# Optimization experiments

Hardware: AMD Instinct MI355X
Metric: run time of the kernel (lower is better)

## Reference

```python
import jax, jax.numpy as jnp
import numpy as np

D_MODEL = 128
D_STATE = 64
D_CONV = 4
EXPAND = 2
HEADDIM = 64
NUM_LAYERS = 2
N_DIR = 6
D_INNER = EXPAND * D_MODEL                    # 256
NHEADS = D_INNER // HEADDIM                   # 4
CONV_DIM = D_INNER + 2 * D_STATE              # 384
D_PROJ = 2 * D_INNER + 2 * D_STATE + NHEADS   # 644
ORDERS = [(0, 1, 2), (0, 2, 1), (1, 0, 2), (1, 2, 0), (2, 0, 1), (2, 1, 0)]


def setup_inputs() -> dict:
    key = jax.random.key(0)
    ks = jax.random.split(key, 10)
    B, L = 1, 16384
    sh = (N_DIR, NUM_LAYERS)
    return {
        'vectors': jax.random.normal(ks[0], (B, L, D_MODEL), jnp.float32),
        'event_coords': jax.random.randint(ks[1], (L, 4), 0, 1024, jnp.int32),
        'ln_w': jnp.ones(sh + (D_MODEL,), jnp.float32),
        'ln_b': jnp.zeros(sh + (D_MODEL,), jnp.float32),
        'in_w': 0.05 * jax.random.normal(ks[2], sh + (D_PROJ, D_MODEL), jnp.float32),
        'conv_w': 0.1 * jax.random.normal(ks[3], sh + (CONV_DIM, D_CONV), jnp.float32),
        'conv_b': jnp.zeros(sh + (CONV_DIM,), jnp.float32),
        'dt_bias': 0.1 * jax.random.normal(ks[4], sh + (NHEADS,), jnp.float32),
        'A_log': jnp.log(jax.random.uniform(ks[5], sh + (NHEADS,), jnp.float32, 1.0, 16.0)),
        'D_skip': jnp.ones(sh + (NHEADS,), jnp.float32),
        'norm_w': jnp.ones(sh + (D_INNER,), jnp.float32),
        'out_w': 0.05 * jax.random.normal(ks[6], sh + (D_MODEL, D_INNER), jnp.float32),
        'fuse_ln_w': jnp.ones((N_DIR * D_MODEL,), jnp.float32),
        'fuse_ln_b': jnp.zeros((N_DIR * D_MODEL,), jnp.float32),
        'fuse_w': 0.05 * jax.random.normal(ks[7], (D_MODEL, N_DIR * D_MODEL), jnp.float32),
        'fuse_b': jnp.zeros((D_MODEL,), jnp.float32),
    }


def _layernorm(x, w, b, eps=1e-5):
    mu = jnp.mean(x, -1, keepdims=True)
    var = jnp.mean((x - mu) ** 2, -1, keepdims=True)
    return (x - mu) * jax.lax.rsqrt(var + eps) * w + b


def _mamba2(x, in_w, conv_w, conv_b, dt_bias, A_log, D_skip, norm_w, out_w):
    # x: [b, l, d_model] -> [b, l, d_model]; Mamba2 (ngroups=1, headdim=64)
    b, l, _ = x.shape
    zxbcdt = jnp.einsum('bld,ed->ble', x, in_w)      # [b,l,644]
    z = zxbcdt[..., :D_INNER]                        # gate [b,l,256]
    xBC = zxbcdt[..., D_INNER:D_INNER + CONV_DIM]    # [b,l,384]
    dt = jax.nn.softplus(zxbcdt[..., D_INNER + CONV_DIM:] + dt_bias)  # [b,l,h]
    # causal depthwise conv over time, then SiLU
    xc = jnp.transpose(xBC, (0, 2, 1))               # [b,c,l]
    xc = jax.lax.conv_general_dilated(
        xc, conv_w[:, None, :], (1,), [(D_CONV - 1, 0)],
        feature_group_count=CONV_DIM, dimension_numbers=('NCH', 'OIH', 'NCH'))
    xBC = jax.nn.silu(jnp.transpose(xc, (0, 2, 1)) + conv_b)
    xs = xBC[..., :D_INNER].reshape(b, l, NHEADS, HEADDIM)   # [b,l,h,p]
    Bm = xBC[..., D_INNER:D_INNER + D_STATE]                 # [b,l,n]
    Cm = xBC[..., D_INNER + D_STATE:]                        # [b,l,n]
    A = -jnp.exp(A_log)                                      # [h]
    dA = jnp.exp(dt * A)                                     # [b,l,h]
    dtx = dt[..., None] * xs                                 # [b,l,h,p]

    def step(h, inp):
        dA_t, dtx_t, B_t, C_t = inp
        h = dA_t[:, :, None, None] * h + dtx_t[..., None] * B_t[:, None, None, :]
        y = jnp.einsum('bn,bhpn->bhp', C_t, h)
        return h, y

    h0 = jnp.zeros((b, NHEADS, HEADDIM, D_STATE), x.dtype)
    _, ys = jax.lax.scan(step, h0, (
        jnp.moveaxis(dA, 1, 0), jnp.moveaxis(dtx, 1, 0),
        jnp.moveaxis(Bm, 1, 0), jnp.moveaxis(Cm, 1, 0)))
    y = jnp.moveaxis(ys, 0, 1) + D_skip[None, None, :, None] * xs  # [b,l,h,p]
    y = y.reshape(b, l, D_INNER)
    # gated RMSNorm (norm_before_gate=False): gate first, then RMSNorm
    y = y * jax.nn.silu(z)
    y = y * jax.lax.rsqrt(jnp.mean(y * y, -1, keepdims=True) + 1e-5) * norm_w
    return jnp.einsum('ble,de->bld', y, out_w)


def _forward(vectors, event_coords, ln_w, ln_b, in_w, conv_w, conv_b, dt_bias,
             A_log, D_skip, norm_w, out_w, fuse_ln_w, fuse_ln_b, fuse_w, fuse_b):
    outs = []
    for d, axes in enumerate(ORDERS):
        keys = [event_coords[:, ax] for ax in reversed(axes)]
        idx = jnp.lexsort(keys)            # lexsort: last key is primary
        inv = jnp.argsort(idx)
        x = vectors[:, idx, :]
        for j in range(NUM_LAYERS):
            x = x + _mamba2(_layernorm(x, ln_w[d, j], ln_b[d, j]),
                            in_w[d, j], conv_w[d, j], conv_b[d, j],
                            dt_bias[d, j], A_log[d, j], D_skip[d, j],
                            norm_w[d, j], out_w[d, j])
        outs.append(x[:, inv, :])
    multi = jnp.concatenate(outs, -1)      # [b,l,6*d_model]
    h = _layernorm(multi, fuse_ln_w, fuse_ln_b)
    h = jnp.einsum('ble,de->bld', h, fuse_w) + fuse_b
    return jax.nn.gelu(h, approximate=False)


def reference(vectors, event_coords, ln_w, ln_b, in_w, conv_w, conv_b, dt_bias,
              A_log, D_skip, norm_w, out_w, fuse_ln_w, fuse_ln_b, fuse_w, fuse_b):
    return _forward(vectors, event_coords, ln_w, ln_b, in_w, conv_w, conv_b,
                    dt_bias, A_log, D_skip, norm_w, out_w,
                    fuse_ln_w, fuse_ln_b, fuse_w, fuse_b)
```

## Files before the change

kernel.cpp:

```cpp
#include <hip/hip_runtime.h>
#include <math.h>

#define LSEQ   16384
#define DM     128
#define DI     256
#define DSTATE 64
#define NH     4
#define HD     64
#define CONVD  384
#define DPROJ  644
#define NDIR   6
#define NCHUNK 256

typedef unsigned short u16;
typedef __attribute__((ext_vector_type(8))) __bf16 bf16x8;
typedef __attribute__((ext_vector_type(4))) float f32x4;

union U8 { uint4 v; u16 h[8]; };

__device__ __constant__ int ORD[6][3] = {{0,1,2},{0,2,1},{1,0,2},{1,2,0},{2,0,1},{2,1,0}};

__device__ __forceinline__ float softplus_f(float x){
  float ax = fabsf(x);
  return fmaxf(x, 0.f) + log1pf(__expf(-ax));
}
__device__ __forceinline__ float silu_f(float x){
  return x / (1.f + __expf(-x));
}
__device__ __forceinline__ u16 f2b(float f){
  unsigned u = __float_as_uint(f);
  unsigned r = (u + 0x7fffu + ((u >> 16) & 1u)) >> 16;
  return (u16)r;
}
__device__ __forceinline__ float b2f(u16 h){
  return __uint_as_float(((unsigned)h) << 16);
}
__device__ __forceinline__ int SWZ(int r, int cb){
  return r*128 + (cb ^ ((r & 7) << 4));
}
__device__ __forceinline__ int SWZ2(int r, int cb){
  return r*256 + (cb ^ ((r & 7) << 4));
}
__device__ __forceinline__ int SWZ4(int r, int cb){
  return r*512 + (cb ^ ((r & 7) << 4));
}

#define NW0 (12*768*128)
#define NW1 (12*128*256)
#define NW2 (128*768)
__global__ __launch_bounds__(256) void k_cvt(const float* __restrict__ in_w,
                                             const float* __restrict__ out_w,
                                             const float* __restrict__ fuse_w,
                                             u16* __restrict__ wi, u16* __restrict__ wo,
                                             u16* __restrict__ wf, int* __restrict__ cursor){
  int i = blockIdx.x*256 + threadIdx.x;
  if (i < NDIR*1024) cursor[i] = 0;
  if (i < NW0){
    int dj = i / (768*128), rem = i % (768*128), r = rem >> 7, c = rem & 127;
    float v = (r < DPROJ) ? in_w[((size_t)dj*DPROJ + r)*128 + c] : 0.f;
    wi[i] = f2b(v);
  } else if (i < NW0 + NW1){
    int k = i - NW0;
    wo[k] = f2b(out_w[k]);
  } else if (i < NW0 + NW1 + NW2){
    int k = i - NW0 - NW1;
    wf[k] = f2b(fuse_w[k]);
  }
}

__global__ __launch_bounds__(256) void k_sort1(const int* __restrict__ coords,
                                               unsigned long long* __restrict__ skey,
                                               int* __restrict__ cursor){
  int i = blockIdx.x*256 + threadIdx.x;
  if (i >= NDIR*LSEQ) return;
  int d = i >> 14, t = i & 16383;
  unsigned k = ((unsigned)coords[t*4 + ORD[d][0]] << 20)
             | ((unsigned)coords[t*4 + ORD[d][1]] << 10)
             |  (unsigned)coords[t*4 + ORD[d][2]];
  skey[i] = ((unsigned long long)k << 14) | (unsigned long long)t;
  atomicAdd(&cursor[(d << 10) + (k >> 20)], 1);
}

__global__ void k_sort_scan(int* __restrict__ cursor, int* __restrict__ starts){
  __shared__ int sh[1024];
  int d = blockIdx.x, t = threadIdx.x;
  int v = cursor[d*1024 + t];
  sh[t] = v; __syncthreads();
  for (int off = 1; off < 1024; off <<= 1){
    int a = (t >= off) ? sh[t-off] : 0;
    __syncthreads();
    sh[t] += a;
    __syncthreads();
  }
  int incl = sh[t], excl = incl - v;
  starts[d*1025 + t] = excl;
  cursor[d*1024 + t] = excl;
  if (t == 1023) starts[d*1025 + 1024] = incl;
}

__global__ __launch_bounds__(256) void k_sort_scatter(const unsigned long long* __restrict__ skey,
                                                      unsigned long long* __restrict__ skey2,
                                                      int* __restrict__ cursor){
  int i = blockIdx.x*256 + threadIdx.x;
  if (i >= NDIR*LSEQ) return;
  int d = i >> 14;
  unsigned long long v = skey[i];
  int b = (int)(v >> 34);
  int pos = atomicAdd(&cursor[(d << 10) + b], 1);
  skey2[(size_t)d*LSEQ + pos] = v;
}

__global__ __launch_bounds__(256) void k_sort_rank(const unsigned long long* __restrict__ skey2,
                                                   const int* __restrict__ starts,
                                                   int* __restrict__ idx){
  int i = blockIdx.x*256 + threadIdx.x;
  if (i >= NDIR*LSEQ) return;
  int d = i >> 14;
  unsigned long long v = skey2[i];
  int b = (int)(v >> 34);
  int s = starts[d*1025 + b], e = starts[d*1025 + b + 1];
  int r = s;
  for (int q = s; q < e; ++q) r += (skey2[(size_t)d*LSEQ + q] < v);
  int orig = (int)(v & 16383ULL);
  idx[(size_t)d*LSEQ + r] = orig;
}

__global__ __launch_bounds__(256) void k_gather(const float* __restrict__ vec, const int* __restrict__ idx,
                                                float* __restrict__ x, int d_base, int nd){
  int i = blockIdx.x*256 + threadIdx.x;
  if (i >= nd*LSEQ*32) return;
  int c4 = i & 31, r = (i >> 5) & 16383, dz = i >> 19;
  int src = idx[(size_t)(d_base+dz)*LSEQ + r];
  ((float4*)x)[((size_t)dz*LSEQ + r)*32 + c4] = ((const float4*)vec)[(size_t)src*32 + c4];
}

__global__ __launch_bounds__(256) void k_inproj(const float* __restrict__ xres,
    const float* __restrict__ lnw, const float* __restrict__ lnb,
    const u16* __restrict__ wbf, const float* __restrict__ dt_bias,
    u16* __restrict__ zbuf, u16* __restrict__ xbc, float* __restrict__ dtb,
    int d_base, int j){
  __shared__ __align__(16) u16 As[64*128];
  __shared__ __align__(16) u16 Bs[128*64];
  int bpair = blockIdx.x, mt = blockIdx.y, dz = blockIdx.z, tid = threadIdx.x;
  int dj = (d_base+dz)*2 + j;
  int l = tid & 63, w = tid >> 6, wr = w >> 1, wc = w & 1;
  if (tid < 128){
    int r = tid >> 1, half = tid & 1;
    const float4* xr = (const float4*)(xres + ((size_t)dz*LSEQ + (size_t)mt*64 + r)*DM + half*64);
    float4 v[16];
    #pragma unroll
    for (int q = 0; q < 16; ++q) v[q] = xr[q];
    float s = 0.f, ss2 = 0.f;
    #pragma unroll
    for (int q = 0; q < 16; ++q){
      s   += v[q].x + v[q].y + v[q].z + v[q].w;
      ss2 += v[q].x*v[q].x + v[q].y*v[q].y + v[q].z*v[q].z + v[q].w*v[q].w;
    }
    s += __shfl_xor(s, 1); ss2 += __shfl_xor(ss2, 1);
    float mu = s*(1.f/128.f);
    float var = ss2*(1.f/128.f) - mu*mu;
    float inv = rsqrtf(var + 1e-5f);
    const float4* w4 = (const float4*)(lnw + (size_t)dj*DM) + half*16;
    const float4* b4 = (const float4*)(lnb + (size_t)dj*DM) + half*16;
    #pragma unroll
    for (int g = 0; g < 8; ++g){
      float4 a = v[2*g], b = v[2*g+1];
      float4 wa = w4[2*g], wb = w4[2*g+1];
      float4 ba = b4[2*g], bb = b4[2*g+1];
      U8 pk;
      pk.h[0] = f2b((a.x-mu)*inv*wa.x + ba.x);
      pk.h[1] = f2b((a.y-mu)*inv*wa.y + ba.y);
      pk.h[2] = f2b((a.z-mu)*inv*wa.z + ba.z);
      pk.h[3] = f2b((a.w-mu)*inv*wa.w + ba.w);
      pk.h[4] = f2b((b.x-mu)*inv*wb.x + bb.x);
      pk.h[5] = f2b((b.y-mu)*inv*wb.y + bb.y);
      pk.h[6] = f2b((b.z-mu)*inv*wb.z + bb.z);
      pk.h[7] = f2b((b.w-mu)*inv*wb.w + bb.w);
      int c0 = half*64 + g*8;
      *(uint4*)((char*)As + SWZ2(r, c0*2)) = pk.v;
    }
  }
  __syncthreads();
  for (int ib = 0; ib < 2; ++ib){
    int bn = bpair*2 + ib;
    const u16* Wd = wbf + (size_t)dj*768*DM + (size_t)bn*128*DM;
    f32x4 acc[2][4] = {};
    for (int kt = 0; kt < 2; ++kt){
      #pragma unroll
      for (int it = 0; it < 4; ++it){
        int idx = it*256 + tid, r = idx >> 3, slot = idx & 7;
        uint4 vb = *(const uint4*)(Wd + (size_t)r*DM + kt*64 + slot*8);
        *(uint4*)((char*)Bs + SWZ(r, slot*16)) = vb;
      }
      __syncthreads();
      #pragma unroll
      for (int ks = 0; ks < 64; ks += 32){
        bf16x8 a[2], b[4];
        int cbb = (ks + (l >> 4)*8)*2;
        int kea = kt*64 + ks + (l >> 4)*8;
        #pragma unroll
        for (int i = 0; i < 2; ++i){
          int ra = wr*32 + i*16 + (l & 15);
          a[i] = *(bf16x8*)((char*)As + SWZ2(ra, kea*2));
        }
        #pragma unroll
        for (int i = 0; i < 4; ++i)
          b[i] = *(bf16x8*)((char*)Bs + SWZ(wc*64 + i*16 + (l & 15), cbb));
        #pragma unroll
        for (int i = 0; i < 2; ++i)
          #pragma unroll
          for (int jn = 0; jn < 4; ++jn)
            acc[i][jn] = __builtin_amdgcn_mfma_f32_16x16x32_bf16(a[i], b[jn], acc[i][jn], 0, 0, 0);
      }
      __syncthreads();
    }
    if (bn < 5){
      #pragma unroll
      for (int i = 0; i < 2; ++i)
        #pragma unroll
        for (int jn = 0; jn < 4; ++jn)
          #pragma unroll
          for (int r = 0; r < 4; ++r){
            int m = wr*32 + i*16 + (l >> 4)*4 + r, n = wc*64 + jn*16 + (l & 15);
            Bs[m*128 + n] = f2b(acc[i][jn][r]);
          }
      __syncthreads();
      int co0 = bn*128;
      u16* dst; int ld;
      if (co0 < 256){ dst = zbuf + ((size_t)dz*LSEQ + (size_t)mt*64)*DI + co0; ld = DI; }
      else         { dst = xbc  + ((size_t)dz*LSEQ + (size_t)mt*64)*CONVD + (co0 - 256); ld = CONVD; }
      #pragma unroll
      for (int it = 0; it < 4; ++it){
        int idx = it*256 + tid, r = idx >> 4, slot = idx & 15;
        uint4 v = *(uint4*)(Bs + r*128 + slot*8);
        *(uint4*)(dst + (size_t)r*ld + slot*8) = v;
      }
      __syncthreads();
    } else {
      #pragma unroll
      for (int i = 0; i < 2; ++i)
        #pragma unroll
        for (int jn = 0; jn < 4; ++jn)
          #pragma unroll
          for (int r = 0; r < 4; ++r){
            int m = wr*32 + i*16 + (l >> 4)*4 + r, n = wc*64 + jn*16 + (l & 15);
            if (n < 4){
              float v = acc[i][jn][r] + dt_bias[dj*4 + n];
              dtb[((size_t)dz*LSEQ + (size_t)mt*64 + m)*4 + n] = softplus_f(v);
            }
          }
    }
  }
}

__global__ __launch_bounds__(256) void k_conv(const u16* __restrict__ xbc, const float* __restrict__ conv_w,
                                              const float* __restrict__ conv_b, u16* __restrict__ xact,
                                              int d_base, int j){
  __shared__ float tile[67][130];
  __shared__ float wsh[128][4];
  __shared__ float bsh[128];
  int dz = blockIdx.x, lb = blockIdx.y*64, cb = blockIdx.z*128;
  int dj = (d_base+dz)*2 + j;
  const u16* src = xbc + (size_t)dz*LSEQ*CONVD + cb;
  for (int e = threadIdx.x; e < 67*16; e += 256){
    int r = e >> 4, cg = e & 15;
    int lrow = lb - 3 + r;
    U8 v;
    if (lrow >= 0) v.v = *(const uint4*)(src + (size_t)lrow*CONVD + cg*8);
    else v.v = make_uint4(0,0,0,0);
    #pragma unroll
    for (int k = 0; k < 8; ++k) tile[r][cg*8 + k] = b2f(v.h[k]);
  }
  if (threadIdx.x < 128){
    int c = threadIdx.x;
    const float* wp = conv_w + ((size_t)dj*CONVD + cb + c)*4;
    wsh[c][0]=wp[0]; wsh[c][1]=wp[1]; wsh[c][2]=wp[2]; wsh[c][3]=wp[3];
    bsh[c] = conv_b[(size_t)dj*CONVD + cb + c];
  }
  __syncthreads();
  for (int e = threadIdx.x; e < 64*16; e += 256){
    int r = e >> 4, cg = e & 15;
    U8 o;
    #pragma unroll
    for (int k = 0; k < 8; ++k){
      int c = cg*8 + k;
      float v = tile[r][c]*wsh[c][0] + tile[r+1][c]*wsh[c][1]
              + tile[r+2][c]*wsh[c][2] + tile[r+3][c]*wsh[c][3] + bsh[c];
      o.h[k] = f2b(silu_f(v));
    }
    *(uint4*)(xact + ((size_t)dz*LSEQ + lb + r)*CONVD + cb + cg*8) = o.v;
  }
}

__global__ __launch_bounds__(256) void k_chunk1(const u16* __restrict__ xact, const float* __restrict__ dtb,
    const float* __restrict__ A_log, const float* __restrict__ Dskip,
    u16* __restrict__ E, u16* __restrict__ y1, float* __restrict__ ltot, int d_base, int j){
  __shared__ __align__(16) u16 sB[4096], sC[4096], sM[4096], sXt[4096], sBw[4096];
  __shared__ float sLl[4][64], sdt[4][64];
  __shared__ float wexp[64];
  int c = blockIdx.x, dz = blockIdx.y, tid = threadIdx.x;
  int dj = (d_base+dz)*2 + j;
  int l = tid & 63, w = tid >> 6, wr = w >> 1, wc = w & 1;
  int mb = wr*32, nb = wc*32;
  int row0 = c*64;
  const u16* xa = xact + ((size_t)dz*LSEQ + row0)*CONVD;
  {
    float4 d4 = *(const float4*)(dtb + ((size_t)dz*LSEQ + row0 + l)*4);
    float dt = (w==0)?d4.x:((w==1)?d4.y:((w==2)?d4.z:d4.w));
    float A = -__expf(A_log[dj*4 + w]);
    float v = dt * A;
    #pragma unroll
    for (int o = 1; o < 64; o <<= 1){ float pv = __shfl_up(v, o); if (l >= o) v += pv; }
    sdt[w][l] = dt; sLl[w][l] = v;
    if (l == 63) ltot[((size_t)(dz*NCHUNK + c))*NH + w] = v;
  }
  #pragma unroll
  for (int it = 0; it < 2; ++it){
    int idx = it*256 + tid, t = idx >> 3, slot = idx & 7;
    uint4 vB = *(const uint4*)(xa + (size_t)t*CONVD + 256 + slot*8);
    uint4 vC = *(const uint4*)(xa + (size_t)t*CONVD + 320 + slot*8);
    *(uint4*)((char*)sB + SWZ(t, slot*16)) = vB;
    *(uint4*)((char*)sC + SWZ(t, slot*16)) = vC;
  }
  __syncthreads();
  f32x4 g[2][2] = {};
  #pragma unroll
  for (int ks = 0; ks < 64; ks += 32){
    bf16x8 a[2], b[2];
    int cb = (ks + (l >> 4)*8)*2;
    #pragma unroll
    for (int i = 0; i < 2; ++i){
      a[i] = *(bf16x8*)((char*)sC + SWZ(mb + i*16 + (l & 15), cb));
      b[i] = *(bf16x8*)((char*)sB + SWZ(nb + i*16 + (l & 15), cb));
    }
    #pragma unroll
    for (int i = 0; i < 2; ++i)
      #pragma unroll
      for (int jn = 0; jn < 2; ++jn)
        g[i][jn] = __builtin_amdgcn_mfma_f32_16x16x32_bf16(a[i], b[jn], g[i][jn], 0, 0, 0);
  }
  for (int h = 0; h < NH; ++h){
    __syncthreads();
    if (tid < 64) wexp[tid] = __expf(sLl[h][63] - sLl[h][tid]) * sdt[h][tid];
    #pragma unroll
    for (int it = 0; it < 2; ++it){
      int idx = it*256 + tid, s = idx >> 3, slot = idx & 7;
      uint4 xv = *(const uint4*)(xa + (size_t)s*CONVD + h*64 + slot*8);
      *(uint4*)((char*)sC + SWZ(s, slot*16)) = xv;
    }
    #pragma unroll
    for (int i = 0; i < 2; ++i)
      #pragma unroll
      for (int jn = 0; jn < 2; ++jn)
        #pragma unroll
        for (int r = 0; r < 4; ++r){
          int t = mb + i*16 + (l >> 4)*4 + r;
          int s = nb + jn*16 + (l & 15);
          float v = (s <= t) ? g[i][jn][r]*__expf(sLl[h][t]-sLl[h][s])*sdt[h][s] : 0.f;
          *(u16*)((char*)sM + SWZ(t, s*2)) = f2b(v);
        }
    __syncthreads();
    #pragma unroll
    for (int it = 0; it < 2; ++it){
      int idx = it*256 + tid, n = idx & 63, so = idx >> 6;
      U8 xo, bo;
      #pragma unroll
      for (int k = 0; k < 8; ++k){
        int s = so*8 + k;
        u16 xv = *(u16*)((char*)sC + SWZ(s, n*2));
        u16 bv = *(u16*)((char*)sB + SWZ(s, n*2));
        xo.h[k] = xv;
        bo.h[k] = f2b(b2f(bv) * wexp[s]);
      }
      *(uint4*)((char*)sXt + SWZ(n, so*16)) = xo.v;
      *(uint4*)((char*)sBw + SWZ(n, so*16)) = bo.v;
    }
    __syncthreads();
    f32x4 y1a[2][2] = {}, ssa[2][2] = {};
    #pragma unroll
    for (int ks = 0; ks < 64; ks += 32){
      int cb = (ks + (l >> 4)*8)*2;
      bf16x8 am[2], ax[2], bx[2], bw2[2];
      #pragma unroll
      for (int i = 0; i < 2; ++i){
        am[i]  = *(bf16x8*)((char*)sM  + SWZ(mb + i*16 + (l & 15), cb));
        ax[i]  = *(bf16x8*)((char*)sXt + SWZ(mb + i*16 + (l & 15), cb));
        bx[i]  = *(bf16x8*)((char*)sXt + SWZ(nb + i*16 + (l & 15), cb));
        bw2[i] = *(bf16x8*)((char*)sBw + SWZ(nb + i*16 + (l & 15), cb));
      }
      #pragma unroll
      for (int i = 0; i < 2; ++i)
        #pragma unroll
        for (int jn = 0; jn < 2; ++jn){
          y1a[i][jn] = __builtin_amdgcn_mfma_f32_16x16x32_bf16(am[i], bx[jn], y1a[i][jn], 0, 0, 0);
          ssa[i][jn] = __builtin_amdgcn_mfma_f32_16x16x32_bf16(ax[i], bw2[jn], ssa[i][jn], 0, 0, 0);
        }
    }
    __syncthreads();
    float dsk = Dskip[dj*NH + h];
    #pragma unroll
    for (int i = 0; i < 2; ++i)
      #pragma unroll
      for (int jn = 0; jn < 2; ++jn)
        #pragma unroll
        for (int r = 0; r < 4; ++r){
          int m = mb + i*16 + (l >> 4)*4 + r, n = nb + jn*16 + (l & 15);
          float xsv = b2f(*(u16*)((char*)sXt + SWZ(n, m*2)));
          *(u16*)((char*)sM  + SWZ(m, n*2)) = f2b(y1a[i][jn][r] + dsk * xsv);
          *(u16*)((char*)sBw + SWZ(m, n*2)) = f2b(ssa[i][jn][r]);
        }
    __syncthreads();
    u16* yr = y1 + ((size_t)dz*LSEQ + row0)*DI + h*64;
    u16* Ep = E + ((size_t)(dz*NCHUNK + c)*NH + h)*4096;
    #pragma unroll
    for (int it = 0; it < 2; ++it){
      int idx = it*256 + tid, r = idx >> 3, slot = idx & 7;
      uint4 vy = *(uint4*)((char*)sM  + SWZ(r, slot*16));
      uint4 ve = *(uint4*)((char*)sBw + SWZ(r, slot*16));
      *(uint4*)(yr + (size_t)r*DI + slot*8) = vy;
      *(uint4*)(Ep + r*64 + slot*8) = ve;
    }
  }
}

__global__ __launch_bounds__(256) void k_seq(u16* __restrict__ E, const float* __restrict__ ltot, int nd){
  int i = blockIdx.x*256 + threadIdx.x;
  if (i >= nd*16384) return;
  int dz = i >> 14, h = (i >> 12) & 3, np = i & 4095;
  const int stride = 16384;
  size_t base = (size_t)dz*NCHUNK*stride + (size_t)h*4096 + np;
  const float* lt = ltot + (size_t)dz*NCHUNK*NH + h;
  u16 eb[16]; float pb[16];
  #pragma unroll
  for (int q = 0; q < 16; ++q){ eb[q] = E[base + (size_t)q*stride]; pb[q] = lt[q*NH]; }
  float carry = 0.f;
  for (int cc = 0; cc < 256; cc += 16){
    u16 e2[16]; float p2[16];
    if (cc + 16 < 256){
      #pragma unroll
      for (int q = 0; q < 16; ++q){
        e2[q] = E[base + (size_t)(cc+16+q)*stride];
        p2[q] = lt[(cc+16+q)*NH];
      }
    }
    #pragma unroll
    for (int q = 0; q < 16; ++q){
      u16 cv = f2b(carry);
      carry = fmaf(__expf(pb[q]), carry, b2f(eb[q]));
      E[base + (size_t)(cc+q)*stride] = cv;
    }
    #pragma unroll
    for (int q = 0; q < 16; ++q){ eb[q] = e2[q]; pb[q] = p2[q]; }
  }
}

__global__ __launch_bounds__(256) void k_chunk2(const u16* __restrict__ xact, const float* __restrict__ dtb,
    const float* __restrict__ A_log, const u16* __restrict__ zbuf, const u16* __restrict__ y1,
    const u16* __restrict__ E, const float* __restrict__ norm_w, const u16* __restrict__ wo,
    float* __restrict__ x, const int* __restrict__ sidx, u16* __restrict__ multi,
    int d_base, int j){
  __shared__ __align__(16) u16 SH[24576];
  u16* sC   = SH;
  u16* sHt  = SH + 4096;
  u16* Ylds = SH + 8192;
  u16* Bs   = SH;
  __shared__ float sLl[4][64];
  __shared__ float nws[256];
  int c = blockIdx.x, dz = blockIdx.y, tid = threadIdx.x;
  int dj = (d_base+dz)*2 + j;
  int l = tid & 63, w = tid >> 6, wr = w >> 1, wc = w & 1;
  int mb = wr*32, nb = wc*32;
  int row0 = c*64;
  const u16* xa = xact + ((size_t)dz*LSEQ + row0)*CONVD;
  if (tid < 64) ((float4*)nws)[tid] = ((const float4*)(norm_w + (size_t)dj*DI))[tid];
  {
    float4 d4 = *(const float4*)(dtb + ((size_t)dz*LSEQ + row0 + l)*4);
    float dt = (w==0)?d4.x:((w==1)?d4.y:((w==2)?d4.z:d4.w));
    float A = -__expf(A_log[dj*4 + w]);
    float v = dt * A;
    #pragma unroll
    for (int o = 1; o < 64; o <<= 1){ float pv = __shfl_up(v, o); if (l >= o) v += pv; }
    sLl[w][l] = v;
  }
  #pragma unroll
  for (int it = 0; it < 2; ++it){
    int idx = it*256 + tid, t = idx >> 3, slot = idx & 7;
    uint4 vC = *(const uint4*)(xa + (size_t)t*CONVD + 320 + slot*8);
    *(uint4*)((char*)sC + SWZ(t, slot*16)) = vC;
  }
  for (int h = 0; h < NH; ++h){
    __syncthreads();
    const u16* Hp = E + ((size_t)(dz*NCHUNK + c)*NH + h)*4096;
    #pragma unroll
    for (int it = 0; it < 2; ++it){
      int idx = it*256 + tid, p = idx >> 3, ng = idx & 7;
      uint4 v = *(const uint4*)(Hp + (size_t)p*64 + ng*8);
      *(uint4*)((char*)sHt + SWZ(p, ng*16)) = v;
    }
    __syncthreads();
    f32x4 acc[2][2] = {};
    #pragma unroll
    for (int ks = 0; ks < 64; ks += 32){
      int cb = (ks + (l >> 4)*8)*2;
      bf16x8 a[2], b[2];
      #pragma unroll
      for (int i = 0; i < 2; ++i){
        a[i] = *(bf16x8*)((char*)sC  + SWZ(mb + i*16 + (l & 15), cb));
        b[i] = *(bf16x8*)((char*)sHt + SWZ(nb + i*16 + (l & 15), cb));
      }
      #pragma unroll
      for (int i = 0; i < 2; ++i)
        #pragma unroll
        for (int jn = 0; jn < 2; ++jn)
          acc[i][jn] = __builtin_amdgcn_mfma_f32_16x16x32_bf16(a[i], b[jn], acc[i][jn], 0, 0, 0);
    }
    #pragma unroll
    for (int i = 0; i < 2; ++i)
      #pragma unroll
      for (int jn = 0; jn < 2; ++jn)
        #pragma unroll
        for (int r = 0; r < 4; ++r){
          int m = mb + i*16 + (l >> 4)*4 + r, n = nb + jn*16 + (l & 15);
          float e = __expf(sLl[h][m]);
          *(u16*)((char*)Ylds + SWZ4(m, (h*64 + n)*2)) = f2b(e * acc[i][jn][r]);
        }
  }
  __syncthreads();
  {
    int r = tid >> 2, q = tid & 3;
    size_t rowbase = ((size_t)dz*LSEQ + row0 + r)*DI + q*64;
    float ssq = 0.f;
    U8 gs[8];
    #pragma unroll
    for (int v = 0; v < 8; ++v){
      U8 y2u; y2u.v = *(uint4*)((char*)Ylds + SWZ4(r, (q*64 + v*8)*2));
      U8 y1u; y1u.v = *(const uint4*)(y1 + rowbase + v*8);
      U8 zu;  zu.v  = *(const uint4*)(zbuf + rowbase + v*8);
      #pragma unroll
      for (int k = 0; k < 8; ++k){
        float gv = (b2f(y1u.h[k]) + b2f(y2u.h[k])) * silu_f(b2f(zu.h[k]));
        ssq += gv*gv;
        gs[v].h[k] = f2b(gv);
      }
    }
    ssq += __shfl_xor(ssq, 1);
    ssq += __shfl_xor(ssq, 2);
    float rr = rsqrtf(ssq * (1.f/256.f) + 1e-5f);
    #pragma unroll
    for (int v = 0; v < 8; ++v){
      U8 o;
      #pragma unroll
      for (int k = 0; k < 8; ++k)
        o.h[k] = f2b(b2f(gs[v].h[k]) * rr * nws[q*64 + v*8 + k]);
      *(uint4*)((char*)Ylds + SWZ4(r, (q*64 + v*8)*2)) = o.v;
    }
  }
  __syncthreads();
  const u16* Bg = wo + (size_t)dj*DM*DI;
  f32x4 acc2[2][4] = {};
  for (int kt = 0; kt < 4; ++kt){
    #pragma unroll
    for (int it = 0; it < 4; ++it){
      int idx = it*256 + tid, r = idx >> 3, slot = idx & 7;
      uint4 vb = *(const uint4*)(Bg + (size_t)r*DI + kt*64 + slot*8);
      *(uint4*)((char*)Bs + SWZ(r, slot*16)) = vb;
    }
    __syncthreads();
    #pragma unroll
    for (int ks = 0; ks < 64; ks += 32){
      bf16x8 a[2], b[4];
      int cb = (ks + (l >> 4)*8)*2;
      int kcol = kt*64 + ks + (l >> 4)*8;
      #pragma unroll
      for (int i = 0; i < 2; ++i)
        a[i] = *(bf16x8*)((char*)Ylds + SWZ4(wr*32 + i*16 + (l & 15), kcol*2));
      #pragma unroll
      for (int i = 0; i < 4; ++i)
        b[i] = *(bf16x8*)((char*)Bs + SWZ(wc*64 + i*16 + (l & 15), cb));
      #pragma unroll
      for (int i = 0; i < 2; ++i)
        #pragma unroll
        for (int jn = 0; jn < 4; ++jn)
          acc2[i][jn] = __builtin_amdgcn_mfma_f32_16x16x32_bf16(a[i], b[jn], acc2[i][jn], 0, 0, 0);
    }
    __syncthreads();
  }
  float* xr = x + ((size_t)dz*LSEQ + row0)*DM;
  if (j == 0){
    #pragma unroll
    for (int i = 0; i < 2; ++i)
      #pragma unroll
      for (int jn = 0; jn < 4; ++jn)
        #pragma unroll
        for (int r = 0; r < 4; ++r){
          int m = wr*32 + i*16 + (l >> 4)*4 + r, n = wc*64 + jn*16 + (l & 15);
          xr[(size_t)m*DM + n] += acc2[i][jn][r];
        }
  } else {
    #pragma unroll
    for (int i = 0; i < 2; ++i)
      #pragma unroll
      for (int jn = 0; jn < 4; ++jn)
        #pragma unroll
        for (int r = 0; r < 4; ++r){
          int m = wr*32 + i*16 + (l >> 4)*4 + r, n = wc*64 + jn*16 + (l & 15);
          float res = xr[(size_t)m*DM + n] + acc2[i][jn][r];
          Bs[m*128 + n] = f2b(res);
        }
    __syncthreads();
    const int* ip = sidx + (size_t)(d_base+dz)*LSEQ + row0;
    #pragma unroll
    for (int it = 0; it < 4; ++it){
      int e = it*256 + tid, r = e >> 4, slot = e & 15;
      int orig = ip[r];
      uint4 v = *(uint4*)(Bs + r*128 + slot*8);
      *(uint4*)(multi + (size_t)orig*768 + (size_t)(d_base+dz)*128 + slot*8) = v;
    }
  }
}

__global__ __launch_bounds__(256) void k_fuse(const u16* __restrict__ multi, const u16* __restrict__ wbf,
                                              const float* __restrict__ lnw, const float* __restrict__ lnb,
                                              const float* __restrict__ fb, float* __restrict__ out){
  __shared__ __align__(16) u16 As[64*64];
  __shared__ __align__(16) u16 Bs[64*64];
  __shared__ float swn[768], sbn[768], smu[64], sinv[64];
  int nh = blockIdx.x, mt = blockIdx.y, tid = threadIdx.x;
  int l = tid & 63, w = tid >> 6, wr = w >> 1, wc = w & 1;
  for (int e = tid; e < 192; e += 256){
    ((float4*)swn)[e] = ((const float4*)lnw)[e];
    ((float4*)sbn)[e] = ((const float4*)lnb)[e];
  }
  {
    int r = tid >> 2, q = tid & 3;
    const u16* row = multi + ((size_t)(mt*64 + r))*768 + q*192;
    float s = 0.f, ss = 0.f;
    #pragma unroll
    for (int v = 0; v < 24; ++v){
      U8 u; u.v = *(const uint4*)(row + v*8);
      #pragma unroll
      for (int k = 0; k < 8; ++k){ float f = b2f(u.h[k]); s += f; ss += f*f; }
    }
    s += __shfl_xor(s, 1); s += __shfl_xor(s, 2);
    ss += __shfl_xor(ss, 1); ss += __shfl_xor(ss, 2);
    if (q == 0){
      float mu = s * (1.f/768.f);
      smu[r] = mu;
      sinv[r] = rsqrtf(ss * (1.f/768.f) - mu*mu + 1e-5f);
    }
  }
  __syncthreads();
  const u16* Ag = multi + (size_t)mt*64*768;
  const u16* Wg = wbf + (size_t)nh*64*768;
  f32x4 acc[2][2] = {};
  for (int kt = 0; kt < 12; ++kt){
    #pragma unroll
    for (int it = 0; it < 2; ++it){
      int e = it*256 + tid, r = e >> 3, slot = e & 7;
      U8 u; u.v = *(const uint4*)(Ag + (size_t)r*768 + kt*64 + slot*8);
      float mu = smu[r], inv = sinv[r];
      U8 o;
      #pragma unroll
      for (int k = 0; k < 8; ++k){
        int col = kt*64 + slot*8 + k;
        o.h[k] = f2b((b2f(u.h[k]) - mu)*inv*swn[col] + sbn[col]);
      }
      *(uint4*)((char*)As + SWZ(r, slot*16)) = o.v;
    }
    #pragma unroll
    for (int it = 0; it < 2; ++it){
      int e = it*256 + tid, r = e >> 3, slot = e & 7;
      uint4 vb = *(const uint4*)(Wg + (size_t)r*768 + kt*64 + slot*8);
      *(uint4*)((char*)Bs + SWZ(r, slot*16)) = vb;
    }
    __syncthreads();
    #pragma unroll
    for (int ks = 0; ks < 64; ks += 32){
      bf16x8 a[2], b[2];
      int cb = (ks + (l >> 4)*8)*2;
      #pragma unroll
      for (int i = 0; i < 2; ++i)
        a[i] = *(bf16x8*)((char*)As + SWZ(wr*32 + i*16 + (l & 15), cb));
      #pragma unroll
      for (int i = 0; i < 2; ++i)
        b[i] = *(bf16x8*)((char*)Bs + SWZ(wc*32 + i*16 + (l & 15), cb));
      #pragma unroll
      for (int i = 0; i < 2; ++i)
        #pragma unroll
        for (int jn = 0; jn < 2; ++jn)
          acc[i][jn] = __builtin_amdgcn_mfma_f32_16x16x32_bf16(a[i], b[jn], acc[i][jn], 0, 0, 0);
    }
    __syncthreads();
  }
  #pragma unroll
  for (int i = 0; i < 2; ++i)
    #pragma unroll
    for (int jn = 0; jn < 2; ++jn)
      #pragma unroll
      for (int r = 0; r < 4; ++r){
        int m = wr*32 + i*16 + (l >> 4)*4 + r;
        int n = nh*64 + wc*32 + jn*16 + (l & 15);
        float v = acc[i][jn][r] + fb[n];
        float gl = 0.5f * v * (1.f + erff(v * 0.70710678118654752f));
        out[(size_t)(mt*64 + m)*DM + n] = gl;
      }
}

extern "C" void kernel_launch(void* const* d_in, const int* in_sizes, int n_in,
                              void* d_out, int out_size, void* d_ws, size_t ws_size,
                              hipStream_t stream){
  (void)in_sizes; (void)n_in; (void)out_size;
  const float* vectors  = (const float*)d_in[0];
  const int*   coords   = (const int*)d_in[1];
  const float* ln_w     = (const float*)d_in[2];
  const float* ln_b     = (const float*)d_in[3];
  const float* in_w     = (const float*)d_in[4];
  const float* conv_w   = (const float*)d_in[5];
  const float* conv_b   = (const float*)d_in[6];
  const float* dt_bias  = (const float*)d_in[7];
  const float* A_log    = (const float*)d_in[8];
  const float* D_skip   = (const float*)d_in[9];
  const float* norm_w   = (const float*)d_in[10];
  const float* out_w    = (const float*)d_in[11];
  const float* fuse_lw  = (const float*)d_in[12];
  const float* fuse_lb  = (const float*)d_in[13];
  const float* fuse_w   = (const float*)d_in[14];
  const float* fuse_b   = (const float*)d_in[15];
  float* out = (float*)d_out;

  char* p = (char*)d_ws;
  auto carve = [&](size_t bytes)->char*{
    char* r = p; p += (bytes + 255) & ~(size_t)255; return r;
  };
  int* idxb = (int*)carve((size_t)NDIR*LSEQ*4);
  unsigned long long* skey  = (unsigned long long*)carve((size_t)NDIR*LSEQ*8);
  unsigned long long* skey2 = (unsigned long long*)carve((size_t)NDIR*LSEQ*8);
  int* starts = (int*)carve((size_t)NDIR*1025*4);
  int* cursor = (int*)carve((size_t)NDIR*1024*4);
  u16* multi = (u16*)carve((size_t)LSEQ*768*2);
  u16* wbf_in   = (u16*)carve((size_t)NW0*2);
  u16* wbf_out  = (u16*)carve((size_t)NW1*2);
  u16* wbf_fuse = (u16*)carve((size_t)NW2*2);

  size_t fixed = (size_t)(p - (char*)d_ws);
  auto need = [&](int nd)->size_t{
    size_t s = 0; auto a = [&](size_t b){ s += (b + 255) & ~(size_t)255; };
    a((size_t)nd*LSEQ*DM*4);
    a((size_t)nd*LSEQ*DI*2);
    a((size_t)nd*LSEQ*CONVD*2);
    a((size_t)nd*LSEQ*CONVD*2);
    a((size_t)nd*LSEQ*NH*4);
    a((size_t)nd*NCHUNK*NH*4);
    a((size_t)nd*LSEQ*DI*2);
    a((size_t)nd*NCHUNK*NH*DSTATE*HD*2);
    return s;
  };
  int nd = 1;
  {
    const int cands[3] = {6, 3, 2};
    for (int ci = 0; ci < 3; ++ci){
      if (fixed + need(cands[ci]) <= ws_size){ nd = cands[ci]; break; }
    }
  }
  if (fixed + need(nd) > ws_size) return;

  float* xbuf = (float*)carve((size_t)nd*LSEQ*DM*4);
  u16*   zbuf = (u16*)carve((size_t)nd*LSEQ*DI*2);
  u16*   xbc  = (u16*)carve((size_t)nd*LSEQ*CONVD*2);
  u16*   xact = (u16*)carve((size_t)nd*LSEQ*CONVD*2);
  float* dtb  = (float*)carve((size_t)nd*LSEQ*NH*4);
  float* ltot = (float*)carve((size_t)nd*NCHUNK*NH*4);
  u16*   y1b  = (u16*)carve((size_t)nd*LSEQ*DI*2);
  u16*   Ebuf = (u16*)carve((size_t)nd*NCHUNK*NH*DSTATE*HD*2);

  k_cvt         <<<(NW0+NW1+NW2+255)/256, 256, 0, stream>>>(in_w, out_w, fuse_w, wbf_in, wbf_out, wbf_fuse, cursor);
  k_sort1       <<<(NDIR*LSEQ + 255)/256, 256, 0, stream>>>(coords, skey, cursor);
  k_sort_scan   <<<NDIR, 1024, 0, stream>>>(cursor, starts);
  k_sort_scatter<<<(NDIR*LSEQ + 255)/256, 256, 0, stream>>>(skey, skey2, cursor);
  k_sort_rank   <<<(NDIR*LSEQ + 255)/256, 256, 0, stream>>>(skey2, starts, idxb);

  for (int d_base = 0; d_base < NDIR; d_base += nd){
    k_gather<<<nd*2048, 256, 0, stream>>>(vectors, idxb, xbuf, d_base, nd);
    for (int j = 0; j < 2; ++j){
      k_inproj<<<dim3(3, LSEQ/64, nd), 256, 0, stream>>>(xbuf, ln_w, ln_b, wbf_in, dt_bias,
                                                         zbuf, xbc, dtb, d_base, j);
      k_conv  <<<dim3(nd, LSEQ/64, 3), 256, 0, stream>>>(xbc, conv_w, conv_b, xact, d_base, j);
      k_chunk1<<<dim3(NCHUNK, nd), 256, 0, stream>>>(xact, dtb, A_log, D_skip,
                                                     Ebuf, y1b, ltot, d_base, j);
      k_seq   <<<(nd*16384 + 255)/256, 256, 0, stream>>>(Ebuf, ltot, nd);
      k_chunk2<<<dim3(NCHUNK, nd), 256, 0, stream>>>(xact, dtb, A_log, zbuf, y1b, Ebuf,
                                                     norm_w, wbf_out, xbuf, idxb, multi, d_base, j);
    }
  }
  k_fuse <<<dim3(2, LSEQ/64), 256, 0, stream>>>(multi, wbf_fuse, fuse_lw, fuse_lb, fuse_b, out);
}
```

Before: 744.4 us.

## Fuse causal depthwise conv into in-projection epilogue with boundary fix-up kernel

The in-projection GEMM epilogue now applies the 4-tap causal conv and SiLU directly to its 64-row tile for the xBC columns. It writes xact and saves the first three and last three pre-conv rows of each tile into a small boundary buffer. A light k_convfix kernel then recomputes the first three rows of every chunk using the previous tile's saved rows. This drops the full bf16 xBC round trip through global memory and the separate conv pass, at the cost of a little extra epilogue work and one more small launch.

```diff
diff --git a/kernel.cpp b/kernel.cpp
--- a/kernel.cpp
+++ b/kernel.cpp
@@ -137,10 +137,13 @@
 __global__ __launch_bounds__(256) void k_inproj(const float* __restrict__ xres,
     const float* __restrict__ lnw, const float* __restrict__ lnb,
     const u16* __restrict__ wbf, const float* __restrict__ dt_bias,
-    u16* __restrict__ zbuf, u16* __restrict__ xbc, float* __restrict__ dtb,
-    int d_base, int j){
+    const float* __restrict__ conv_w, const float* __restrict__ conv_b,
+    u16* __restrict__ zbuf, u16* __restrict__ xact, u16* __restrict__ bnd,
+    float* __restrict__ dtb, int d_base, int j){
   __shared__ __align__(16) u16 As[64*128];
   __shared__ __align__(16) u16 Bs[128*64];
+  __shared__ float cwsh[128][4];
+  __shared__ float cbsh[128];
   int bpair = blockIdx.x, mt = blockIdx.y, dz = blockIdx.z, tid = threadIdx.x;
   int dj = (d_base+dz)*2 + j;
   int l = tid & 63, w = tid >> 6, wr = w >> 1, wc = w & 1;
@@ -214,7 +217,7 @@
       }
       __syncthreads();
     }
-    if (bn < 5){
+    if (bn < 2){
       #pragma unroll
       for (int i = 0; i < 2; ++i)
         #pragma unroll
@@ -225,15 +228,59 @@
             Bs[m*128 + n] = f2b(acc[i][jn][r]);
           }
       __syncthreads();
-      int co0 = bn*128;
-      u16* dst; int ld;
-      if (co0 < 256){ dst = zbuf + ((size_t)dz*LSEQ + (size_t)mt*64)*DI + co0; ld = DI; }
-      else         { dst = xbc  + ((size_t)dz*LSEQ + (size_t)mt*64)*CONVD + (co0 - 256); ld = CONVD; }
+      u16* dst = zbuf + ((size_t)dz*LSEQ + (size_t)mt*64)*DI + bn*128;
       #pragma unroll
       for (int it = 0; it < 4; ++it){
         int idx = it*256 + tid, r = idx >> 4, slot = idx & 15;
         uint4 v = *(uint4*)(Bs + r*128 + slot*8);
-        *(uint4*)(dst + (size_t)r*ld + slot*8) = v;
+        *(uint4*)(dst + (size_t)r*DI + slot*8) = v;
+      }
+      __syncthreads();
+    } else if (bn < 5){
+      int xco0 = bn*128 - 256;
+      #pragma unroll
+      for (int i = 0; i < 2; ++i)
+        #pragma unroll
+        for (int jn = 0; jn < 4; ++jn)
+          #pragma unroll
+          for (int r = 0; r < 4; ++r){
+            int m = wr*32 + i*16 + (l >> 4)*4 + r, n = wc*64 + jn*16 + (l & 15);
+            Bs[m*128 + n] = f2b(acc[i][jn][r]);
+          }
+      if (tid < 128){
+        const float* wp = conv_w + ((size_t)dj*CONVD + xco0 + tid)*4;
+        cwsh[tid][0]=wp[0]; cwsh[tid][1]=wp[1]; cwsh[tid][2]=wp[2]; cwsh[tid][3]=wp[3];
+        cbsh[tid] = conv_b[(size_t)dj*CONVD + xco0 + tid];
+      }
+      __syncthreads();
+      u16* bt = bnd + ((size_t)(dz*NCHUNK + mt)*6)*CONVD + xco0;
+      u16* xdst = xact + ((size_t)dz*LSEQ + (size_t)mt*64)*CONVD + xco0;
+      #pragma unroll
+      for (int it = 0; it < 4; ++it){
+        int idx = it*256 + tid, r = idx >> 4, slot = idx & 15;
+        int colbase = slot*8;
+        if (r < 3){
+          uint4 v = *(uint4*)(Bs + r*128 + colbase);
+          *(uint4*)(bt + (size_t)r*CONVD + colbase) = v;
+        } else {
+          if (r >= 61){
+            uint4 v = *(uint4*)(Bs + r*128 + colbase);
+            *(uint4*)(bt + (size_t)(r-58)*CONVD + colbase) = v;
+          }
+          U8 tp[4];
+          #pragma unroll
+          for (int k = 0; k < 4; ++k)
+            tp[k].v = *(uint4*)(Bs + (r-3+k)*128 + colbase);
+          U8 o;
+          #pragma unroll
+          for (int k2 = 0; k2 < 8; ++k2){
+            int c = colbase + k2;
+            float v = b2f(tp[0].h[k2])*cwsh[c][0] + b2f(tp[1].h[k2])*cwsh[c][1]
+                    + b2f(tp[2].h[k2])*cwsh[c][2] + b2f(tp[3].h[k2])*cwsh[c][3] + cbsh[c];
+            o.h[k2] = f2b(silu_f(v));
+          }
+          *(uint4*)(xdst + (size_t)r*CONVD + colbase) = o.v;
+        }
       }
       __syncthreads();
     } else {
@@ -253,43 +300,34 @@
   }
 }
 
-__global__ __launch_bounds__(256) void k_conv(const u16* __restrict__ xbc, const float* __restrict__ conv_w,
-                                              const float* __restrict__ conv_b, u16* __restrict__ xact,
-                                              int d_base, int j){
-  __shared__ float tile[67][130];
-  __shared__ float wsh[128][4];
-  __shared__ float bsh[128];
-  int dz = blockIdx.x, lb = blockIdx.y*64, cb = blockIdx.z*128;
+__global__ __launch_bounds__(256) void k_convfix(const u16* __restrict__ bnd,
+    const float* __restrict__ conv_w, const float* __restrict__ conv_b,
+    u16* __restrict__ xact, int d_base, int j){
+  int mt = blockIdx.x, dz = blockIdx.y, tid = threadIdx.x;
   int dj = (d_base+dz)*2 + j;
-  const u16* src = xbc + (size_t)dz*LSEQ*CONVD + cb;
-  for (int e = threadIdx.x; e < 67*16; e += 256){
-    int r = e >> 4, cg = e & 15;
-    int lrow = lb - 3 + r;
-    U8 v;
-    if (lrow >= 0) v.v = *(const uint4*)(src + (size_t)lrow*CONVD + cg*8);
-    else v.v = make_uint4(0,0,0,0);
-    #pragma unroll
-    for (int k = 0; k < 8; ++k) tile[r][cg*8 + k] = b2f(v.h[k]);
-  }
-  if (threadIdx.x < 128){
-    int c = threadIdx.x;
-    const float* wp = conv_w + ((size_t)dj*CONVD + cb + c)*4;
-    wsh[c][0]=wp[0]; wsh[c][1]=wp[1]; wsh[c][2]=wp[2]; wsh[c][3]=wp[3];
-    bsh[c] = conv_b[(size_t)dj*CONVD + cb + c];
-  }
-  __syncthreads();
-  for (int e = threadIdx.x; e < 64*16; e += 256){
-    int r = e >> 4, cg = e & 15;
-    U8 o;
-    #pragma unroll
-    for (int k = 0; k < 8; ++k){
-      int c = cg*8 + k;
-      float v = tile[r][c]*wsh[c][0] + tile[r+1][c]*wsh[c][1]
-              + tile[r+2][c]*wsh[c][2] + tile[r+3][c]*wsh[c][3] + bsh[c];
-      o.h[k] = f2b(silu_f(v));
-    }
-    *(uint4*)(xact + ((size_t)dz*LSEQ + lb + r)*CONVD + cb + cg*8) = o.v;
-  }
+  if (tid >= 144) return;
+  int r = tid / 48, cg = tid % 48;
+  int col = cg*8;
+  const u16* bcur  = bnd + ((size_t)(dz*NCHUNK + mt)*6)*CONVD;
+  const u16* bprev = bnd + ((size_t)(dz*NCHUNK + mt - 1)*6)*CONVD;
+  U8 tp[4];
+  #pragma unroll
+  for (int k = 0; k < 4; ++k){
+    int grow = r - 3 + k;
+    if (grow >= 0) tp[k].v = *(const uint4*)(bcur + (size_t)grow*CONVD + col);
+    else if (mt > 0) tp[k].v = *(const uint4*)(bprev + (size_t)(6 + grow)*CONVD + col);
+    else tp[k].v = make_uint4(0,0,0,0);
+  }
+  U8 o;
+  #pragma unroll
+  for (int k2 = 0; k2 < 8; ++k2){
+    int c = col + k2;
+    const float* wp = conv_w + ((size_t)dj*CONVD + c)*4;
+    float v = b2f(tp[0].h[k2])*wp[0] + b2f(tp[1].h[k2])*wp[1]
+            + b2f(tp[2].h[k2])*wp[2] + b2f(tp[3].h[k2])*wp[3] + conv_b[(size_t)dj*CONVD + c];
+    o.h[k2] = f2b(silu_f(v));
+  }
+  *(uint4*)(xact + ((size_t)dz*LSEQ + (size_t)mt*64 + r)*CONVD + col) = o.v;
 }
 
 __global__ __launch_bounds__(256) void k_chunk1(const u16* __restrict__ xact, const float* __restrict__ dtb,
@@ -748,7 +786,7 @@
     a((size_t)nd*LSEQ*DM*4);
     a((size_t)nd*LSEQ*DI*2);
     a((size_t)nd*LSEQ*CONVD*2);
-    a((size_t)nd*LSEQ*CONVD*2);
+    a((size_t)nd*NCHUNK*6*CONVD*2);
     a((size_t)nd*LSEQ*NH*4);
     a((size_t)nd*NCHUNK*NH*4);
     a((size_t)nd*LSEQ*DI*2);
@@ -766,8 +804,8 @@
 
   float* xbuf = (float*)carve((size_t)nd*LSEQ*DM*4);
   u16*   zbuf = (u16*)carve((size_t)nd*LSEQ*DI*2);
-  u16*   xbc  = (u16*)carve((size_t)nd*LSEQ*CONVD*2);
   u16*   xact = (u16*)carve((size_t)nd*LSEQ*CONVD*2);
+  u16*   bnd  = (u16*)carve((size_t)nd*NCHUNK*6*CONVD*2);
   float* dtb  = (float*)carve((size_t)nd*LSEQ*NH*4);
   float* ltot = (float*)carve((size_t)nd*NCHUNK*NH*4);
   u16*   y1b  = (u16*)carve((size_t)nd*LSEQ*DI*2);
@@ -783,8 +821,8 @@
     k_gather<<<nd*2048, 256, 0, stream>>>(vectors, idxb, xbuf, d_base, nd);
     for (int j = 0; j < 2; ++j){
       k_inproj<<<dim3(3, LSEQ/64, nd), 256, 0, stream>>>(xbuf, ln_w, ln_b, wbf_in, dt_bias,
-                                                         zbuf, xbc, dtb, d_base, j);
-      k_conv  <<<dim3(nd, LSEQ/64, 3), 256, 0, stream>>>(xbc, conv_w, conv_b, xact, d_base, j);
+                                                         conv_w, conv_b, zbuf, xact, bnd, dtb, d_base, j);
+      k_convfix<<<dim3(NCHUNK, nd), 256, 0, stream>>>(bnd, conv_w, conv_b, xact, d_base, j);
       k_chunk1<<<dim3(NCHUNK, nd), 256, 0, stream>>>(xact, dtb, A_log, D_skip,
                                                      Ebuf, y1b, ltot, d_base, j);
       k_seq   <<<(nd*16384 + 255)/256, 256, 0, stream>>>(Ebuf, ltot, nd);
```

New measurement: 725.4 us. -2.6%, faster.
